# Kernel optimization log

Hardware: AMD Instinct MI355X
Metric: run time of the kernel (lower is better)

Reference implementation:

```python
import jax, jax.numpy as jnp
import numpy as np

# Config (matches init_kwargs)
B, T, N = 32, 512, 1024
FT, FS = 16, 32                 # max_time_F, max_space_F
NCH = FT * FS                   # n_channels = 512
MULT = 2
DIN = NCH * MULT                # input_dim = 1024
H = 1024                        # hidden_size
NCLS = 1                        # n_cls_tokens
NP = (T // FT) * (N // FS)      # n_patches = 1024
SCALE = float(H) ** 0.5         # config.scale is None -> hidden_size**0.5


def setup_inputs() -> dict:
    key = jax.random.key(0)
    k0, k1, k2, k3 = jax.random.split(key, 4)
    s = 0.02
    return {
        "spikes": jax.random.normal(k0, (B, T, N), dtype=jnp.float32),
        "W_embed": jax.random.normal(k1, (DIN, NCH), dtype=jnp.float32) * s,
        "b_embed": jnp.zeros((DIN,), dtype=jnp.float32),
        "cls_tokens": jnp.zeros((1, NCLS, DIN), dtype=jnp.float32),
        "W_proj": jax.random.normal(k2, (H, DIN), dtype=jnp.float32) * s,
        "b_proj": jnp.zeros((H,), dtype=jnp.float32),
        "pos_table": jax.random.normal(k3, (NP + NCLS, H), dtype=jnp.float32) * s,
    }


def reference(spikes, W_embed, b_embed, cls_tokens, W_proj, b_proj, pos_table):
    Bsz = spikes.shape[0]
    # Patchify: replaces the double python loop with one reshape/transpose.
    # [B,T,N] -> [B, T/FT, FT, N/FS, FS] -> [B, T/FT, N/FS, FT, FS] -> [B, NP, NCH]
    # flatten order (time-major within patch) matches torch's .flatten(1) on [B,FT,FS].
    patches = spikes.reshape(Bsz, T // FT, FT, N // FS, FS)
    patches = patches.transpose(0, 1, 3, 2, 4).reshape(Bsz, NP, NCH)
    # embed_spikes (linear)
    x = jnp.einsum("bpc,dc->bpd", patches, W_embed) + b_embed
    # prepend cls tokens
    cls = jnp.broadcast_to(cls_tokens, (Bsz, NCLS, DIN))
    x = jnp.concatenate([cls, x], axis=1)
    # act * scale, then projection
    x = jax.nn.gelu(x, approximate=False) * SCALE
    x = jnp.einsum("bpd,hd->bph", x, W_proj) + b_proj
    # positional embedding: stamps are arange, so direct table add
    stamp = jnp.broadcast_to(
        jnp.arange(NP + NCLS, dtype=jnp.int32)[None, :], (Bsz, NP + NCLS)
    )
    mask = jnp.ones((Bsz, NP + NCLS), dtype=jnp.int32)
    x = x + pos_table[None, :, :]
    # dropout p=0.0 -> identity
    return (x, mask, stamp)
```

## Files before the change

### kernel.cpp

```cpp
#include <hip/hip_runtime.h>
#include <stdint.h>


typedef __attribute__((ext_vector_type(8))) short bf16x8;
typedef __attribute__((ext_vector_type(4))) float f32x4;

__device__ __forceinline__ unsigned short f2bf(float f) {
  union { float f; unsigned u; } v; v.f = f;
  const unsigned u = v.u;
  return (unsigned short)((u + 0x7fffu + ((u >> 16) & 1u)) >> 16);
}

__device__ __forceinline__ float gelu_exact(float x) {
  return 0.5f * x * (1.0f + erff(x * 0.70710678118654752440f));
}

__device__ __forceinline__ void gl_lds16(const unsigned short* g, unsigned short* l) {
  __builtin_amdgcn_global_load_lds(
      (const __attribute__((address_space(1))) unsigned int*)g,
      (__attribute__((address_space(3))) unsigned int*)l, 16, 0, 0);
}


__global__ void cast_f32_bf16(const float* __restrict__ src,
                              unsigned short* __restrict__ dst, int n) {
  const int i = blockIdx.x * 256 + threadIdx.x;
  if (i < n) dst[i] = f2bf(src[i]);
}

__global__ void patchify(const float* __restrict__ spikes,
                         unsigned short* __restrict__ P) {
  const int idx = blockIdx.x * 256 + threadIdx.x;
  const int m = idx >> 7;
  const int c = (idx & 127) << 2;
  const int b = m >> 10, p = m & 1023;
  const int pt = p >> 5, ps = p & 31;
  const int ft = c >> 5, fs = c & 31;
  const float4 v = *(const float4*)(spikes +
      (size_t)(((b << 9) + pt * 16 + ft) << 10) + ps * 32 + fs);
  ushort4 o;
  o.x = f2bf(v.x); o.y = f2bf(v.y); o.z = f2bf(v.z); o.w = f2bf(v.w);
  *(ushort4*)(P + (size_t)m * 512 + c) = o;
}

__global__ void g0_and_pad(const float* __restrict__ cls,
                           unsigned short* __restrict__ G) {
  const int i = blockIdx.x * 256 + threadIdx.x;
  G[(size_t)32800 * 1024 + i] = 0;
  if (i < 1024) {
    const unsigned short bv = f2bf(gelu_exact(cls[i]) * 32.0f);
    for (int b = 0; b < 32; ++b) G[(size_t)(b * 1025) * 1024 + i] = bv;
  }
}

__global__ void mask_stamp(float* __restrict__ out) {
  const int i = blockIdx.x * 256 + threadIdx.x;
  if (i < 32800) {
    out[33587200 + i] = 1.0f;
    out[33587200 + 32800 + i] = (float)(i % 1025);
  }
}

template <int K, bool GELU_EPI>
__global__ __launch_bounds__(256) void gemm_bt(
    const unsigned short* __restrict__ A, const unsigned short* __restrict__ B,
    const float* __restrict__ bias, unsigned short* __restrict__ Cg,
    float* __restrict__ Cf, const float* __restrict__ pos, int Mvalid) {
  __shared__ __align__(16) unsigned short lsA[128 * 64];
  __shared__ __align__(16) unsigned short lsB[128 * 64];
  const int tid = threadIdx.x;
  const int lane = tid & 63;
  const int w = tid >> 6;
  const int quad = lane >> 4;
  const int l16 = lane & 15;
  const int rowStart = blockIdx.y * 128;
  const int colStart = blockIdx.x * 128;
  const int wm = (w >> 1) * 64;
  const int wn = (w & 1) * 64;

  f32x4 acc[4][4];
  const f32x4 z = {0.f, 0.f, 0.f, 0.f};
#pragma unroll
  for (int i = 0; i < 4; ++i)
#pragma unroll
    for (int j = 0; j < 4; ++j) acc[i][j] = z;

  const int sr = w * 32 + (lane >> 3);
  const int kc = (lane & 7) * 8;

  for (int k0 = 0; k0 < K; k0 += 64) {
    __syncthreads();
#pragma unroll
    for (int s = 0; s < 4; ++s) {
      const int r = sr + s * 8;
      gl_lds16(A + (size_t)(rowStart + r) * K + (k0 + kc), lsA + r * 64 + kc);
      gl_lds16(B + (size_t)(colStart + r) * K + (k0 + kc), lsB + r * 64 + kc);
    }
    __syncthreads();
#pragma unroll
    for (int kk = 0; kk < 64; kk += 32) {
      bf16x8 af[4], bfr[4];
#pragma unroll
      for (int i = 0; i < 4; ++i)
        af[i] = *(const bf16x8*)(lsA + (wm + i * 16 + l16) * 64 + kk + quad * 8);
#pragma unroll
      for (int j = 0; j < 4; ++j)
        bfr[j] = *(const bf16x8*)(lsB + (wn + j * 16 + l16) * 64 + kk + quad * 8);
#pragma unroll
      for (int i = 0; i < 4; ++i)
#pragma unroll
        for (int j = 0; j < 4; ++j)
          acc[i][j] = __builtin_amdgcn_mfma_f32_16x16x32_bf16(af[i], bfr[j],
                                                              acc[i][j], 0, 0, 0);
    }
  }

#pragma unroll
  for (int i = 0; i < 4; ++i) {
    const int rb = rowStart + wm + i * 16 + quad * 4;
#pragma unroll
    for (int j = 0; j < 4; ++j) {
      const int gc = colStart + wn + j * 16 + l16;
      const float bv = bias[gc];
#pragma unroll
      for (int r = 0; r < 4; ++r) {
        const int row = rb + r;
        float v = acc[i][j][r] + bv;
        if (GELU_EPI) {
          v = gelu_exact(v) * 32.0f;
          const int grow = row + (row >> 10) + 1;
          Cg[(size_t)grow * 1024 + gc] = f2bf(v);
        } else {
          if (row < Mvalid) {
            const int p = row % 1025;
            Cf[(size_t)row * 1024 + gc] = v + pos[(size_t)p * 1024 + gc];
          }
        }
      }
    }
  }
}


extern "C" void kernel_launch(void* const* d_in, const int* in_sizes, int n_in,
                              void* d_out, int out_size, void* d_ws, size_t ws_size,
                              hipStream_t stream) {
  const float* spikes  = (const float*)d_in[0];
  const float* W_embed = (const float*)d_in[1];
  const float* b_embed = (const float*)d_in[2];
  const float* cls     = (const float*)d_in[3];
  const float* W_proj  = (const float*)d_in[4];
  const float* b_proj  = (const float*)d_in[5];
  const float* pos     = (const float*)d_in[6];
  float* out = (float*)d_out;

  char* ws = (char*)d_ws;
  unsigned short* P  = (unsigned short*)(ws);
  unsigned short* G  = (unsigned short*)(ws + 33554432);
  unsigned short* WE = (unsigned short*)(ws + 100925440);
  unsigned short* WP = (unsigned short*)(ws + 101974016);

  hipLaunchKernelGGL(cast_f32_bf16, dim3(2048), dim3(256), 0, stream, W_embed, WE, 524288);
  hipLaunchKernelGGL(cast_f32_bf16, dim3(4096), dim3(256), 0, stream, W_proj, WP, 1048576);
  hipLaunchKernelGGL(patchify, dim3(16384), dim3(256), 0, stream, spikes, P);
  hipLaunchKernelGGL(g0_and_pad, dim3(384), dim3(256), 0, stream, cls, G);
  hipLaunchKernelGGL(mask_stamp, dim3(129), dim3(256), 0, stream, out);

  hipLaunchKernelGGL((gemm_bt<512, true>), dim3(8, 256), dim3(256), 0, stream,
                     P, WE, b_embed, G, (float*)nullptr, (const float*)nullptr, 0);
  hipLaunchKernelGGL((gemm_bt<1024, false>), dim3(8, 257), dim3(256), 0, stream,
                     G, WP, b_proj, (unsigned short*)nullptr, out, pos, 32800);
}
```

Before: 443.8 us.

## Swizzle LDS layout and remap GEMM blocks for XCD-local L2 reuse

Both GEMMs now launch a flat 1D grid. Each block's tile is remapped so that blocks landing on the same XCD (block id mod 8) work on a contiguous range of row-blocks across all eight column-blocks, which is meant to improve L2 reuse of the A operand. The LDS tile layout also gets an XOR swizzle on its 16-byte chunks, applied on both the global_load_lds writes and the fragment reads, to cut LDS bank conflicts. The extra index arithmetic is small, but the mapping hardcodes the grid shape, including a special case for the 257th row-block.

```diff
diff --git a/kernel.cpp b/kernel.cpp
--- a/kernel.cpp
+++ b/kernel.cpp
@@ -61,7 +61,7 @@
   }
 }
 
-template <int K, bool GELU_EPI>
+template <int K, bool GELU_EPI, int ROWBLKS>
 __global__ __launch_bounds__(256) void gemm_bt(
     const unsigned short* __restrict__ A, const unsigned short* __restrict__ B,
     const float* __restrict__ bias, unsigned short* __restrict__ Cg,
@@ -73,8 +73,15 @@
   const int w = tid >> 6;
   const int quad = lane >> 4;
   const int l16 = lane & 15;
-  const int rowStart = blockIdx.y * 128;
-  const int colStart = blockIdx.x * 128;
+
+  const int L = blockIdx.x;
+  const int xcd = L & 7;
+  const int j = L >> 3;
+  int rowBlk, colBlk;
+  if (ROWBLKS > 256 && j >= 256) { rowBlk = 256; colBlk = xcd; }
+  else { rowBlk = xcd * 32 + (j >> 3); colBlk = j & 7; }
+  const int rowStart = rowBlk * 128;
+  const int colStart = colBlk * 128;
   const int wm = (w >> 1) * 64;
   const int wn = (w & 1) * 64;
 
@@ -83,35 +90,42 @@
 #pragma unroll
   for (int i = 0; i < 4; ++i)
 #pragma unroll
-    for (int j = 0; j < 4; ++j) acc[i][j] = z;
+    for (int j2 = 0; j2 < 4; ++j2) acc[i][j2] = z;
 
-  const int sr = w * 32 + (lane >> 3);
-  const int kc = (lane & 7) * 8;
+  const int g0 = w * 256 + lane;
 
   for (int k0 = 0; k0 < K; k0 += 64) {
     __syncthreads();
 #pragma unroll
     for (int s = 0; s < 4; ++s) {
-      const int r = sr + s * 8;
-      gl_lds16(A + (size_t)(rowStart + r) * K + (k0 + kc), lsA + r * 64 + kc);
-      gl_lds16(B + (size_t)(colStart + r) * K + (k0 + kc), lsB + r * 64 + kc);
+      const int g = g0 + s * 64;
+      const int r = g >> 3;
+      const int slot = g & 7;
+      const int kc = (slot ^ (r & 7)) * 8;
+      gl_lds16(A + (size_t)(rowStart + r) * K + (k0 + kc), lsA + r * 64 + slot * 8);
+      gl_lds16(B + (size_t)(colStart + r) * K + (k0 + kc), lsB + r * 64 + slot * 8);
     }
     __syncthreads();
 #pragma unroll
     for (int kk = 0; kk < 64; kk += 32) {
       bf16x8 af[4], bfr[4];
+      const int kcb = (kk >> 3) + quad;
 #pragma unroll
-      for (int i = 0; i < 4; ++i)
-        af[i] = *(const bf16x8*)(lsA + (wm + i * 16 + l16) * 64 + kk + quad * 8);
+      for (int i = 0; i < 4; ++i) {
+        const int r = wm + i * 16 + l16;
+        af[i] = *(const bf16x8*)(lsA + r * 64 + (kcb ^ (r & 7)) * 8);
+      }
 #pragma unroll
-      for (int j = 0; j < 4; ++j)
-        bfr[j] = *(const bf16x8*)(lsB + (wn + j * 16 + l16) * 64 + kk + quad * 8);
+      for (int j2 = 0; j2 < 4; ++j2) {
+        const int r = wn + j2 * 16 + l16;
+        bfr[j2] = *(const bf16x8*)(lsB + r * 64 + (kcb ^ (r & 7)) * 8);
+      }
 #pragma unroll
       for (int i = 0; i < 4; ++i)
 #pragma unroll
-        for (int j = 0; j < 4; ++j)
-          acc[i][j] = __builtin_amdgcn_mfma_f32_16x16x32_bf16(af[i], bfr[j],
-                                                              acc[i][j], 0, 0, 0);
+        for (int j2 = 0; j2 < 4; ++j2)
+          acc[i][j2] = __builtin_amdgcn_mfma_f32_16x16x32_bf16(af[i], bfr[j2],
+                                                               acc[i][j2], 0, 0, 0);
     }
   }
 
@@ -119,13 +133,13 @@
   for (int i = 0; i < 4; ++i) {
     const int rb = rowStart + wm + i * 16 + quad * 4;
 #pragma unroll
-    for (int j = 0; j < 4; ++j) {
-      const int gc = colStart + wn + j * 16 + l16;
+    for (int j2 = 0; j2 < 4; ++j2) {
+      const int gc = colStart + wn + j2 * 16 + l16;
       const float bv = bias[gc];
 #pragma unroll
       for (int r = 0; r < 4; ++r) {
         const int row = rb + r;
-        float v = acc[i][j][r] + bv;
+        float v = acc[i][j2][r] + bv;
         if (GELU_EPI) {
           v = gelu_exact(v) * 32.0f;
           const int grow = row + (row >> 10) + 1;
@@ -166,8 +180,8 @@
   hipLaunchKernelGGL(g0_and_pad, dim3(384), dim3(256), 0, stream, cls, G);
   hipLaunchKernelGGL(mask_stamp, dim3(129), dim3(256), 0, stream, out);
 
-  hipLaunchKernelGGL((gemm_bt<512, true>), dim3(8, 256), dim3(256), 0, stream,
+  hipLaunchKernelGGL((gemm_bt<512, true, 256>), dim3(2048), dim3(256), 0, stream,
                      P, WE, b_embed, G, (float*)nullptr, (const float*)nullptr, 0);
-  hipLaunchKernelGGL((gemm_bt<1024, false>), dim3(8, 257), dim3(256), 0, stream,
+  hipLaunchKernelGGL((gemm_bt<1024, false, 257>), dim3(2056), dim3(256), 0, stream,
                      G, WP, b_proj, (unsigned short*)nullptr, out, pos, 32800);
 }
```

Result: faster. 426.8 us (-3.8%).
